# Kernel optimization log

Measured on AMD Instinct MI355X. Metric: run time of the kernel, lower is better.

The kernel has to match this reference:

```python
import jax, jax.numpy as jnp
import numpy as np

B, S, D, H = 2, 2048, 1024, 16
DK = D // H


def setup_inputs() -> dict:
    key = jax.random.key(0)
    ks = jax.random.split(key, 11)
    sc = 0.02
    return {
        "q": jax.random.normal(ks[0], (B, S, D), jnp.float32),
        "k": jax.random.normal(ks[1], (B, S, D), jnp.float32),
        "v": jax.random.normal(ks[2], (B, S, D), jnp.float32),
        "mask": jnp.ones((1, 1, S, S), jnp.int32),
        "w_q": jax.random.normal(ks[3], (D, D), jnp.float32) * sc,
        "b_q": jnp.zeros((D,), jnp.float32),
        "w_k": jax.random.normal(ks[4], (D, D), jnp.float32) * sc,
        "b_k": jnp.zeros((D,), jnp.float32),
        "w_v": jax.random.normal(ks[5], (D, D), jnp.float32) * sc,
        "b_v": jnp.zeros((D,), jnp.float32),
        "w_o": jax.random.normal(ks[6], (D, D), jnp.float32) * sc,
        "b_o": jnp.zeros((D,), jnp.float32),
    }


def reference(q, k, v, mask, w_q, b_q, w_k, b_k, w_v, b_v, w_o, b_o):
    # projections (torch Linear: x @ W.T + b)
    Q = q @ w_q.T + b_q
    K = k @ w_k.T + b_k
    V = v @ w_v.T + b_v
    # [B,S,D] -> [B,H,S,DK]
    Q = Q.reshape(B, S, H, DK).transpose(0, 2, 1, 3)
    K = K.reshape(B, S, H, DK).transpose(0, 2, 1, 3)
    V = V.reshape(B, S, H, DK).transpose(0, 2, 1, 3)
    scores = jnp.einsum('bhqd,bhkd->bhqk', Q, K) / jnp.sqrt(jnp.float32(DK))
    scores = jnp.where(mask == 0, jnp.float32(-1e9), scores)
    attn = jax.nn.softmax(scores, axis=-1)  # dropout p=0.0 -> identity
    X = jnp.einsum('bhqk,bhkd->bhqd', attn, V)
    X = X.transpose(0, 2, 1, 3).reshape(B, S, D)
    return X @ w_o.T + b_o
```

## Files before the change

### kernel.cpp

```cpp
#include <hip/hip_runtime.h>
#include <cstdint>
#include <cstddef>


typedef __attribute__((ext_vector_type(8))) short short8;
typedef __attribute__((ext_vector_type(4))) float float4v;
typedef __attribute__((ext_vector_type(4))) unsigned short us4;

#define DEV __device__ __forceinline__
#define MFMA16(a, b, c) __builtin_amdgcn_mfma_f32_16x16x32_bf16((a), (b), (c), 0, 0, 0)

DEV unsigned short f2bf(float f) {
  union { float f; unsigned u; } c; c.f = f;
  unsigned u = c.u + 0x7fffu + ((c.u >> 16) & 1u);
  return (unsigned short)(u >> 16);
}

DEV void async16(const void* g, void* l) {
  __builtin_amdgcn_global_load_lds(
      (__attribute__((address_space(1))) void*)(uintptr_t)g,
      (__attribute__((address_space(3))) void*)l, 16, 0, 0);
}

struct CvtJob { const float* src; unsigned short* dst; int n; int mode; };
struct CvtArgs { CvtJob job[8]; };

__global__ __launch_bounds__(256) void cvt_bf16_kernel(CvtArgs args) {
  CvtJob j = args.job[blockIdx.y];
  int i = (blockIdx.x * 256 + threadIdx.x) * 8;
  if (i >= j.n) return;
  if (j.mode == 0) {
    float4v a = *(const float4v*)(j.src + i);
    float4v b = *(const float4v*)(j.src + i + 4);
    short8 o;
#pragma unroll
    for (int t = 0; t < 4; ++t) { o[t] = (short)f2bf(a[t]); o[t + 4] = (short)f2bf(b[t]); }
    *(short8*)(j.dst + i) = o;
  } else {
    const int* mi = (const int*)j.src + i;
    int4 a = ((const int4*)mi)[0], b = ((const int4*)mi)[1];
    unsigned bits = (a.x != 0 ? 1u : 0) | (a.y != 0 ? 2u : 0) | (a.z != 0 ? 4u : 0) |
                    (a.w != 0 ? 8u : 0) | (b.x != 0 ? 16u : 0) | (b.y != 0 ? 32u : 0) |
                    (b.z != 0 ? 64u : 0) | (b.w != 0 ? 128u : 0);
    unsigned long long w = (unsigned long long)bits << ((threadIdx.x & 7) * 8);
    w |= __shfl_xor(w, 1);
    w |= __shfl_xor(w, 2);
    w |= __shfl_xor(w, 4);
    if ((threadIdx.x & 7) == 0) ((unsigned long long*)j.dst)[i >> 6] = w;
  }
}

__global__ __launch_bounds__(128) void mask_flags_kernel(const unsigned long long* __restrict__ mb,
                                                         unsigned int* __restrict__ flags) {
  int qb = blockIdx.x >> 5, kt = blockIdx.x & 31;
  int t = threadIdx.x;
  unsigned long long w = mb[(size_t)(qb * 128 + t) * 32 + kt];
  unsigned long long b = __ballot(w == ~0ULL);
  __shared__ unsigned int sh[2];
  if ((t & 63) == 0) sh[t >> 6] = (b == ~0ULL) ? 1u : 0u;
  __syncthreads();
  if (t == 0) flags[blockIdx.x] = sh[0] & sh[1];
}

struct GemmJob {
  const unsigned short* A; const unsigned short* W; const float* bias;
  void* out; float scale; int mode;
};
struct GemmArgs { GemmJob job[3]; };

__global__ __launch_bounds__(256, 2) void gemm128_kernel(GemmArgs args) {
  const GemmJob jb = args.job[blockIdx.z];
  const int tid = threadIdx.x;
  const int wave = tid >> 6, lane = tid & 63, lk = lane & 15, quad = lane >> 4;
  const int wm = wave >> 1, wn = wave & 1;
  const int m0 = blockIdx.y * 128, n0 = blockIdx.x * 128;

  __shared__ unsigned short As[128 * 32];
  __shared__ unsigned short Bs[128 * 32];

  float4v acc[4][4] = {};

  const char* Ag = (const char*)jb.A + (size_t)m0 * 2048;
  const char* Wg = (const char*)jb.W + (size_t)n0 * 2048;

#pragma unroll 1
  for (int kk = 0; kk < 32; ++kk) {
    __syncthreads();
    const int kbyte = kk * 64;
#pragma unroll
    for (int i = 0; i < 2; ++i) {
      int o = (wave * 2 + i) * 1024 + lane * 16;
      int r = o >> 6, cb = o & 63;
      async16(Ag + (size_t)r * 2048 + kbyte + cb, (char*)As + (wave * 2 + i) * 1024);
      async16(Wg + (size_t)r * 2048 + kbyte + cb, (char*)Bs + (wave * 2 + i) * 1024);
    }
    __builtin_amdgcn_s_waitcnt(0);
    __syncthreads();

    short8 af[4];
#pragma unroll
    for (int mt = 0; mt < 4; ++mt)
      af[mt] = *(const short8*)(&As[(wm * 64 + mt * 16 + lk) * 32 + quad * 8]);
#pragma unroll
    for (int nt = 0; nt < 4; ++nt) {
      short8 bf = *(const short8*)(&Bs[(wn * 64 + nt * 16 + lk) * 32 + quad * 8]);
#pragma unroll
      for (int mt = 0; mt < 4; ++mt)
        acc[mt][nt] = MFMA16(af[mt], bf, acc[mt][nt]);
    }
  }

  if (jb.mode == 0) {
    unsigned short* outp = (unsigned short*)jb.out;
#pragma unroll
    for (int nt = 0; nt < 4; ++nt) {
      int n = n0 + wn * 64 + nt * 16 + lk;
      float bn = jb.bias[n];
      int h = n >> 6, d = n & 63;
#pragma unroll
      for (int mt = 0; mt < 4; ++mt) {
#pragma unroll
        for (int r = 0; r < 4; ++r) {
          int m = m0 + wm * 64 + mt * 16 + quad * 4 + r;
          int b = m >> 11, s = m & 2047;
          float v = (acc[mt][nt][r] + bn) * jb.scale;
          outp[((size_t)((b * 16 + h) * 2048 + s) << 6) + d] = f2bf(v);
        }
      }
    }
  } else {
    unsigned short* outp = (unsigned short*)jb.out;
#pragma unroll
    for (int nt = 0; nt < 4; ++nt) {
      int n = n0 + wn * 64 + nt * 16 + lk;
      float bn = jb.bias[n];
      int h = n >> 6, d = n & 63;
#pragma unroll
      for (int mt = 0; mt < 4; ++mt) {
        int m = m0 + wm * 64 + mt * 16 + quad * 4;
        int b = m >> 11, s = m & 2047;
        us4 pk;
#pragma unroll
        for (int r = 0; r < 4; ++r) pk[r] = f2bf(acc[mt][nt][r] + bn);
        *(us4*)(&outp[((size_t)((b * 16 + h) * 64 + d) << 11) + s]) = pk;
      }
    }
  }
}

__global__ __launch_bounds__(256, 2) void gemm_out64_kernel(
    const unsigned short* __restrict__ A, const unsigned short* __restrict__ W,
    const float* __restrict__ bias, float* __restrict__ out) {
  const int tid = threadIdx.x;
  const int wave = tid >> 6, lane = tid & 63, lk = lane & 15, quad = lane >> 4;
  const int wm = wave >> 1, wn = wave & 1;
  const int m0 = blockIdx.y * 64, n0 = blockIdx.x * 128;

  __shared__ unsigned short As[64 * 32];
  __shared__ unsigned short Bs[128 * 32];

  float4v acc[2][4] = {};

  const char* Ag = (const char*)A + (size_t)m0 * 2048;
  const char* Wg = (const char*)W + (size_t)n0 * 2048;

#pragma unroll 1
  for (int kk = 0; kk < 32; ++kk) {
    __syncthreads();
    const int kbyte = kk * 64;
    {
      int o = wave * 1024 + lane * 16;
      int r = o >> 6, cb = o & 63;
      async16(Ag + (size_t)r * 2048 + kbyte + cb, (char*)As + wave * 1024);
    }
#pragma unroll
    for (int i = 0; i < 2; ++i) {
      int o = (wave * 2 + i) * 1024 + lane * 16;
      int r = o >> 6, cb = o & 63;
      async16(Wg + (size_t)r * 2048 + kbyte + cb, (char*)Bs + (wave * 2 + i) * 1024);
    }
    __builtin_amdgcn_s_waitcnt(0);
    __syncthreads();

    short8 af[2];
#pragma unroll
    for (int mt = 0; mt < 2; ++mt)
      af[mt] = *(const short8*)(&As[(wm * 32 + mt * 16 + lk) * 32 + quad * 8]);
#pragma unroll
    for (int nt = 0; nt < 4; ++nt) {
      short8 bf = *(const short8*)(&Bs[(wn * 64 + nt * 16 + lk) * 32 + quad * 8]);
#pragma unroll
      for (int mt = 0; mt < 2; ++mt)
        acc[mt][nt] = MFMA16(af[mt], bf, acc[mt][nt]);
    }
  }

#pragma unroll
  for (int nt = 0; nt < 4; ++nt) {
    int n = n0 + wn * 64 + nt * 16 + lk;
    float bn = bias[n];
#pragma unroll
    for (int mt = 0; mt < 2; ++mt) {
#pragma unroll
      for (int r = 0; r < 4; ++r) {
        int m = m0 + wm * 32 + mt * 16 + quad * 4 + r;
        out[(size_t)m * 1024 + n] = acc[mt][nt][r] + bn;
      }
    }
  }
}

__global__ __launch_bounds__(256, 2) void attn_kernel(
    const unsigned short* __restrict__ Qp, const unsigned short* __restrict__ Kp,
    const unsigned short* __restrict__ Vtp, const unsigned int* __restrict__ flags,
    const unsigned long long* __restrict__ mbits, unsigned short* __restrict__ Xout) {
  __shared__ unsigned short Qs[128 * 64];
  __shared__ unsigned short Ks[2][64 * 64];
  __shared__ unsigned short Vts[2][64 * 64];
  __shared__ unsigned short Ps[128 * 72];
  __shared__ float lsum[128];

  const int tid = threadIdx.x, wave = tid >> 6, lane = tid & 63;
  const int lk = lane & 15, quad = lane >> 4;
  const int bh = blockIdx.y, q0 = blockIdx.x * 128;
  const size_t cbase = (size_t)bh * (2048 * 64);
  const int r8 = lane >> 3, gs = lane & 7;

#pragma unroll
  for (int i = 0; i < 4; ++i) {
    int row = wave * 32 + i * 8 + r8;
    int g = gs ^ (row & 7);
    async16(Qp + cbase + (size_t)(q0 + row) * 64 + g * 8,
            (char*)Qs + (wave * 32 + i * 8) * 128);
  }
#pragma unroll
  for (int i = 0; i < 2; ++i) {
    int row = wave * 16 + i * 8 + r8;
    int g = gs ^ (row & 7);
    async16(Kp + cbase + (size_t)row * 64 + g * 8, (char*)&Ks[0][0] + (wave * 16 + i * 8) * 128);
    async16(Vtp + cbase + (size_t)row * 2048 + g * 8, (char*)&Vts[0][0] + (wave * 16 + i * 8) * 128);
  }
  __builtin_amdgcn_s_waitcnt(0);
  __syncthreads();

  short8 qf[2][2];
#pragma unroll
  for (int mt = 0; mt < 2; ++mt)
#pragma unroll
    for (int ks = 0; ks < 2; ++ks) {
      int row = wave * 32 + mt * 16 + lk;
      int gg = (ks * 4 + quad) ^ (lk & 7);
      qf[mt][ks] = *(const short8*)(&Qs[row * 64 + gg * 8]);
    }

  float rs[8];
#pragma unroll
  for (int i = 0; i < 8; ++i) rs[i] = 0.f;
  float4v O[4][2] = {};

#pragma unroll 1
  for (int kt = 0; kt < 32; ++kt) {
    const int cur = kt & 1;
    if (kt < 31) {
#pragma unroll
      for (int i = 0; i < 2; ++i) {
        int row = wave * 16 + i * 8 + r8;
        int g = gs ^ (row & 7);
        async16(Kp + cbase + (size_t)((kt + 1) * 64 + row) * 64 + g * 8,
                (char*)&Ks[cur ^ 1][0] + (wave * 16 + i * 8) * 128);
        async16(Vtp + cbase + (size_t)row * 2048 + (kt + 1) * 64 + g * 8,
                (char*)&Vts[cur ^ 1][0] + (wave * 16 + i * 8) * 128);
      }
    }

    float4v sacc[2][4] = {};
#pragma unroll
    for (int nt = 0; nt < 4; ++nt) {
      int krow = nt * 16 + lk;
      short8 kb0 = *(const short8*)(&Ks[cur][krow * 64 + ((quad) ^ (lk & 7)) * 8]);
      short8 kb1 = *(const short8*)(&Ks[cur][krow * 64 + ((4 + quad) ^ (lk & 7)) * 8]);
#pragma unroll
      for (int mt = 0; mt < 2; ++mt) {
        sacc[mt][nt] = MFMA16(qf[mt][0], kb0, sacc[mt][nt]);
        sacc[mt][nt] = MFMA16(qf[mt][1], kb1, sacc[mt][nt]);
      }
    }

    if (__builtin_expect(flags[blockIdx.x * 32 + kt] == 0, 0)) {
#pragma unroll
      for (int i = 0; i < 8; ++i) {
        int row = q0 + wave * 32 + (i >> 2) * 16 + quad * 4 + (i & 3);
        unsigned long long w = mbits[(size_t)row * 32 + kt];
#pragma unroll
        for (int nt = 0; nt < 4; ++nt)
          if (!((w >> (nt * 16 + lk)) & 1ULL))
            sacc[i >> 2][nt][i & 3] = -__builtin_inff();
      }
    }

#pragma unroll
    for (int mt = 0; mt < 2; ++mt)
#pragma unroll
      for (int nt = 0; nt < 4; ++nt)
#pragma unroll
        for (int r = 0; r < 4; ++r) {
          float p = __expf(sacc[mt][nt][r]);
          unsigned pu = __float_as_uint(p);
          rs[mt * 4 + r] += __uint_as_float(pu & 0xffff0000u);
          Ps[(wave * 32 + mt * 16 + quad * 4 + r) * 72 + nt * 16 + lk] =
              (unsigned short)(pu >> 16);
        }

    short8 pb[2][2];
#pragma unroll
    for (int qt = 0; qt < 2; ++qt)
#pragma unroll
      for (int ks = 0; ks < 2; ++ks)
        pb[qt][ks] = *(const short8*)(&Ps[(wave * 32 + qt * 16 + lk) * 72 + ks * 32 + quad * 8]);
#pragma unroll
    for (int dt = 0; dt < 4; ++dt) {
      int drow = dt * 16 + lk;
      short8 va0 = *(const short8*)(&Vts[cur][drow * 64 + ((quad) ^ (lk & 7)) * 8]);
      short8 va1 = *(const short8*)(&Vts[cur][drow * 64 + ((4 + quad) ^ (lk & 7)) * 8]);
#pragma unroll
      for (int qt = 0; qt < 2; ++qt) {
        O[dt][qt] = MFMA16(va0, pb[qt][0], O[dt][qt]);
        O[dt][qt] = MFMA16(va1, pb[qt][1], O[dt][qt]);
      }
    }

    __builtin_amdgcn_s_waitcnt(0x0f70);
    __syncthreads();
  }

#pragma unroll
  for (int i = 0; i < 8; ++i) {
    float s = rs[i];
    s += __shfl_xor(s, 1); s += __shfl_xor(s, 2);
    s += __shfl_xor(s, 4); s += __shfl_xor(s, 8);
    rs[i] = s;
  }
  if (lk == 0) {
#pragma unroll
    for (int i = 0; i < 8; ++i)
      lsum[wave * 32 + (i >> 2) * 16 + quad * 4 + (i & 3)] = rs[i];
  }
  __syncthreads();
  float linv[2];
#pragma unroll
  for (int qt = 0; qt < 2; ++qt) linv[qt] = 1.f / lsum[wave * 32 + qt * 16 + lk];

  const int b = bh >> 4, h = bh & 15;
#pragma unroll
  for (int dt = 0; dt < 4; ++dt)
#pragma unroll
    for (int qt = 0; qt < 2; ++qt) {
      int s = q0 + wave * 32 + qt * 16 + lk;
      us4 pk;
#pragma unroll
      for (int rr = 0; rr < 4; ++rr) pk[rr] = f2bf(O[dt][qt][rr] * linv[qt]);
      *(us4*)(&Xout[((size_t)(b * 2048 + s)) * 1024 + h * 64 + dt * 16 + quad * 4]) = pk;
    }
}

extern "C" void kernel_launch(void* const* d_in, const int* in_sizes, int n_in,
                              void* d_out, int out_size, void* d_ws, size_t ws_size,
                              hipStream_t stream) {
  const float* q   = (const float*)d_in[0];
  const float* k   = (const float*)d_in[1];
  const float* v   = (const float*)d_in[2];
  const int*   msk = (const int*)d_in[3];
  const float* w_q = (const float*)d_in[4];
  const float* b_q = (const float*)d_in[5];
  const float* w_k = (const float*)d_in[6];
  const float* b_k = (const float*)d_in[7];
  const float* w_v = (const float*)d_in[8];
  const float* b_v = (const float*)d_in[9];
  const float* w_o = (const float*)d_in[10];
  const float* b_o = (const float*)d_in[11];

  char* ws = (char*)d_ws;
  const size_t MB = (size_t)1 << 20;
  unsigned short* q_bf  = (unsigned short*)(ws + 0 * MB);
  unsigned short* k_bf  = (unsigned short*)(ws + 8 * MB);
  unsigned short* v_bf  = (unsigned short*)(ws + 16 * MB);
  unsigned short* wq_bf = (unsigned short*)(ws + 24 * MB);
  unsigned short* wk_bf = (unsigned short*)(ws + 26 * MB);
  unsigned short* wv_bf = (unsigned short*)(ws + 28 * MB);
  unsigned short* wo_bf = (unsigned short*)(ws + 30 * MB);
  unsigned short* Qp    = (unsigned short*)(ws + 32 * MB);
  unsigned short* Kp    = (unsigned short*)(ws + 40 * MB);
  unsigned short* Vtp   = (unsigned short*)(ws + 48 * MB);
  unsigned short* Xa    = (unsigned short*)(ws + 56 * MB);
  unsigned long long* mb = (unsigned long long*)(ws + 64 * MB);
  unsigned int* mflags   = (unsigned int*)(ws + 64 * MB + (512 << 10));

  CvtArgs ca;
  ca.job[0] = { q,   q_bf,  4096 * 1024, 0 };
  ca.job[1] = { k,   k_bf,  4096 * 1024, 0 };
  ca.job[2] = { v,   v_bf,  4096 * 1024, 0 };
  ca.job[3] = { w_q, wq_bf, 1024 * 1024, 0 };
  ca.job[4] = { w_k, wk_bf, 1024 * 1024, 0 };
  ca.job[5] = { w_v, wv_bf, 1024 * 1024, 0 };
  ca.job[6] = { w_o, wo_bf, 1024 * 1024, 0 };
  ca.job[7] = { (const float*)msk, (unsigned short*)mb, 2048 * 2048, 1 };
  cvt_bf16_kernel<<<dim3(2048, 8), 256, 0, stream>>>(ca);

  mask_flags_kernel<<<dim3(512), 128, 0, stream>>>(mb, mflags);

  GemmArgs ga;
  ga.job[0] = { q_bf, wq_bf, b_q, (void*)Qp,  0.125f, 0 };
  ga.job[1] = { k_bf, wk_bf, b_k, (void*)Kp,  1.0f,   0 };
  ga.job[2] = { v_bf, wv_bf, b_v, (void*)Vtp, 1.0f,   2 };
  gemm128_kernel<<<dim3(8, 32, 3), 256, 0, stream>>>(ga);

  attn_kernel<<<dim3(16, 32), 256, 0, stream>>>(Qp, Kp, Vtp, mflags, mb, Xa);

  gemm_out64_kernel<<<dim3(8, 64), 256, 0, stream>>>(Xa, wo_bf, b_o, (float*)d_out);
}
```

Before: 254.6 us.

## Shrink attention Q tile to 64 rows, single-buffer K/V, raise occupancy

The attention kernel now processes 64 query rows per block instead of 128, doubling the grid. K and V tiles are single-buffered, and the launch bound asks for 4 blocks per CU to hide latency through occupancy rather than through software prefetch. The MFMA operand orientation is swapped so each lane owns a query column, which makes the row-sum reduction a pair of shuffles instead of an LDS pass. The mask-flag kernel moves to 64-row granularity to match. The trade-offs are twice the K/V global traffic, no load/compute overlap inside a block, and output written as scalar 2-byte stores.

```diff
diff --git a/kernel.cpp b/kernel.cpp
--- a/kernel.cpp
+++ b/kernel.cpp
@@ -50,16 +50,12 @@
   }
 }
 
-__global__ __launch_bounds__(128) void mask_flags_kernel(const unsigned long long* __restrict__ mb,
-                                                         unsigned int* __restrict__ flags) {
+__global__ __launch_bounds__(64) void mask_flags_kernel(const unsigned long long* __restrict__ mb,
+                                                        unsigned int* __restrict__ flags) {
   int qb = blockIdx.x >> 5, kt = blockIdx.x & 31;
-  int t = threadIdx.x;
-  unsigned long long w = mb[(size_t)(qb * 128 + t) * 32 + kt];
+  unsigned long long w = mb[(size_t)(qb * 64 + threadIdx.x) * 32 + kt];
   unsigned long long b = __ballot(w == ~0ULL);
-  __shared__ unsigned int sh[2];
-  if ((t & 63) == 0) sh[t >> 6] = (b == ~0ULL) ? 1u : 0u;
-  __syncthreads();
-  if (t == 0) flags[blockIdx.x] = sh[0] & sh[1];
+  if (threadIdx.x == 0) flags[blockIdx.x] = (b == ~0ULL) ? 1u : 0u;
 }
 
 struct GemmJob {
@@ -210,156 +206,120 @@
   }
 }
 
-__global__ __launch_bounds__(256, 2) void attn_kernel(
+__global__ __launch_bounds__(256, 4) void attn_kernel(
     const unsigned short* __restrict__ Qp, const unsigned short* __restrict__ Kp,
     const unsigned short* __restrict__ Vtp, const unsigned int* __restrict__ flags,
     const unsigned long long* __restrict__ mbits, unsigned short* __restrict__ Xout) {
-  __shared__ unsigned short Qs[128 * 64];
-  __shared__ unsigned short Ks[2][64 * 64];
-  __shared__ unsigned short Vts[2][64 * 64];
-  __shared__ unsigned short Ps[128 * 72];
-  __shared__ float lsum[128];
+  __shared__ unsigned short Qs[64 * 64];
+  __shared__ unsigned short Ks[64 * 64];
+  __shared__ unsigned short Vts[64 * 64];
+  __shared__ unsigned short Ps[64 * 72];
 
   const int tid = threadIdx.x, wave = tid >> 6, lane = tid & 63;
   const int lk = lane & 15, quad = lane >> 4;
-  const int bh = blockIdx.y, q0 = blockIdx.x * 128;
+  const int bh = blockIdx.y, q0 = blockIdx.x * 64;
   const size_t cbase = (size_t)bh * (2048 * 64);
   const int r8 = lane >> 3, gs = lane & 7;
-
-#pragma unroll
-  for (int i = 0; i < 4; ++i) {
-    int row = wave * 32 + i * 8 + r8;
-    int g = gs ^ (row & 7);
-    async16(Qp + cbase + (size_t)(q0 + row) * 64 + g * 8,
-            (char*)Qs + (wave * 32 + i * 8) * 128);
-  }
+  const int sw = lk & 7;
+
 #pragma unroll
   for (int i = 0; i < 2; ++i) {
     int row = wave * 16 + i * 8 + r8;
     int g = gs ^ (row & 7);
-    async16(Kp + cbase + (size_t)row * 64 + g * 8, (char*)&Ks[0][0] + (wave * 16 + i * 8) * 128);
-    async16(Vtp + cbase + (size_t)row * 2048 + g * 8, (char*)&Vts[0][0] + (wave * 16 + i * 8) * 128);
-  }
-  __builtin_amdgcn_s_waitcnt(0);
-  __syncthreads();
-
-  short8 qf[2][2];
-#pragma unroll
-  for (int mt = 0; mt < 2; ++mt)
-#pragma unroll
-    for (int ks = 0; ks < 2; ++ks) {
-      int row = wave * 32 + mt * 16 + lk;
-      int gg = (ks * 4 + quad) ^ (lk & 7);
-      qf[mt][ks] = *(const short8*)(&Qs[row * 64 + gg * 8]);
-    }
-
-  float rs[8];
-#pragma unroll
-  for (int i = 0; i < 8; ++i) rs[i] = 0.f;
-  float4v O[4][2] = {};
+    async16(Qp + cbase + (size_t)(q0 + row) * 64 + g * 8,
+            (char*)Qs + (wave * 16 + i * 8) * 128);
+  }
+  __builtin_amdgcn_s_waitcnt(0x0f70);
+
+  short8 qf[2];
+#pragma unroll
+  for (int ks = 0; ks < 2; ++ks) {
+    int row = wave * 16 + lk;
+    int gg = (ks * 4 + quad) ^ (row & 7);
+    qf[ks] = *(const short8*)(&Qs[row * 64 + gg * 8]);
+  }
+
+  float rsum = 0.f;
+  float4v O[4] = {};
 
 #pragma unroll 1
   for (int kt = 0; kt < 32; ++kt) {
-    const int cur = kt & 1;
-    if (kt < 31) {
-#pragma unroll
-      for (int i = 0; i < 2; ++i) {
-        int row = wave * 16 + i * 8 + r8;
-        int g = gs ^ (row & 7);
-        async16(Kp + cbase + (size_t)((kt + 1) * 64 + row) * 64 + g * 8,
-                (char*)&Ks[cur ^ 1][0] + (wave * 16 + i * 8) * 128);
-        async16(Vtp + cbase + (size_t)row * 2048 + (kt + 1) * 64 + g * 8,
-                (char*)&Vts[cur ^ 1][0] + (wave * 16 + i * 8) * 128);
+    __syncthreads();
+#pragma unroll
+    for (int i = 0; i < 2; ++i) {
+      int row = wave * 16 + i * 8 + r8;
+      int g = gs ^ (row & 7);
+      async16(Kp + cbase + (size_t)(kt * 64 + row) * 64 + g * 8,
+              (char*)Ks + (wave * 16 + i * 8) * 128);
+      async16(Vtp + cbase + (size_t)row * 2048 + kt * 64 + g * 8,
+              (char*)Vts + (wave * 16 + i * 8) * 128);
+    }
+    __builtin_amdgcn_s_waitcnt(0x0f70);
+    __syncthreads();
+
+    float4v sacc[4] = {};
+#pragma unroll
+    for (int kt4 = 0; kt4 < 4; ++kt4) {
+      int krow = kt4 * 16 + lk;
+      short8 ka0 = *(const short8*)(&Ks[krow * 64 + ((quad) ^ sw) * 8]);
+      short8 ka1 = *(const short8*)(&Ks[krow * 64 + ((4 + quad) ^ sw) * 8]);
+      sacc[kt4] = MFMA16(ka0, qf[0], sacc[kt4]);
+      sacc[kt4] = MFMA16(ka1, qf[1], sacc[kt4]);
+    }
+
+    if (__builtin_expect(flags[blockIdx.x * 32 + kt] == 0, 0)) {
+      unsigned long long w = mbits[(size_t)(q0 + wave * 16 + lk) * 32 + kt];
+#pragma unroll
+      for (int kt4 = 0; kt4 < 4; ++kt4)
+#pragma unroll
+        for (int r = 0; r < 4; ++r)
+          if (!((w >> (kt4 * 16 + quad * 4 + r)) & 1ULL))
+            sacc[kt4][r] = -__builtin_inff();
+    }
+
+#pragma unroll
+    for (int kt4 = 0; kt4 < 4; ++kt4) {
+      us4 pk;
+#pragma unroll
+      for (int r = 0; r < 4; ++r) {
+        float p = __expf(sacc[kt4][r]);
+        unsigned pu = __float_as_uint(p);
+        rsum += __uint_as_float(pu & 0xffff0000u);
+        pk[r] = (unsigned short)(pu >> 16);
       }
-    }
-
-    float4v sacc[2][4] = {};
-#pragma unroll
-    for (int nt = 0; nt < 4; ++nt) {
-      int krow = nt * 16 + lk;
-      short8 kb0 = *(const short8*)(&Ks[cur][krow * 64 + ((quad) ^ (lk & 7)) * 8]);
-      short8 kb1 = *(const short8*)(&Ks[cur][krow * 64 + ((4 + quad) ^ (lk & 7)) * 8]);
-#pragma unroll
-      for (int mt = 0; mt < 2; ++mt) {
-        sacc[mt][nt] = MFMA16(qf[mt][0], kb0, sacc[mt][nt]);
-        sacc[mt][nt] = MFMA16(qf[mt][1], kb1, sacc[mt][nt]);
-      }
-    }
-
-    if (__builtin_expect(flags[blockIdx.x * 32 + kt] == 0, 0)) {
-#pragma unroll
-      for (int i = 0; i < 8; ++i) {
-        int row = q0 + wave * 32 + (i >> 2) * 16 + quad * 4 + (i & 3);
-        unsigned long long w = mbits[(size_t)row * 32 + kt];
-#pragma unroll
-        for (int nt = 0; nt < 4; ++nt)
-          if (!((w >> (nt * 16 + lk)) & 1ULL))
-            sacc[i >> 2][nt][i & 3] = -__builtin_inff();
-      }
-    }
-
-#pragma unroll
-    for (int mt = 0; mt < 2; ++mt)
-#pragma unroll
-      for (int nt = 0; nt < 4; ++nt)
-#pragma unroll
-        for (int r = 0; r < 4; ++r) {
-          float p = __expf(sacc[mt][nt][r]);
-          unsigned pu = __float_as_uint(p);
-          rs[mt * 4 + r] += __uint_as_float(pu & 0xffff0000u);
-          Ps[(wave * 32 + mt * 16 + quad * 4 + r) * 72 + nt * 16 + lk] =
-              (unsigned short)(pu >> 16);
-        }
-
-    short8 pb[2][2];
-#pragma unroll
-    for (int qt = 0; qt < 2; ++qt)
-#pragma unroll
-      for (int ks = 0; ks < 2; ++ks)
-        pb[qt][ks] = *(const short8*)(&Ps[(wave * 32 + qt * 16 + lk) * 72 + ks * 32 + quad * 8]);
+      *(us4*)(&Ps[(wave * 16 + lk) * 72 + kt4 * 16 + quad * 4]) = pk;
+    }
+
+    short8 pa[2];
+#pragma unroll
+    for (int ks = 0; ks < 2; ++ks)
+      pa[ks] = *(const short8*)(&Ps[(wave * 16 + lk) * 72 + ks * 32 + quad * 8]);
 #pragma unroll
     for (int dt = 0; dt < 4; ++dt) {
       int drow = dt * 16 + lk;
-      short8 va0 = *(const short8*)(&Vts[cur][drow * 64 + ((quad) ^ (lk & 7)) * 8]);
-      short8 va1 = *(const short8*)(&Vts[cur][drow * 64 + ((4 + quad) ^ (lk & 7)) * 8]);
-#pragma unroll
-      for (int qt = 0; qt < 2; ++qt) {
-        O[dt][qt] = MFMA16(va0, pb[qt][0], O[dt][qt]);
-        O[dt][qt] = MFMA16(va1, pb[qt][1], O[dt][qt]);
-      }
-    }
-
-    __builtin_amdgcn_s_waitcnt(0x0f70);
-    __syncthreads();
-  }
-
-#pragma unroll
-  for (int i = 0; i < 8; ++i) {
-    float s = rs[i];
-    s += __shfl_xor(s, 1); s += __shfl_xor(s, 2);
-    s += __shfl_xor(s, 4); s += __shfl_xor(s, 8);
-    rs[i] = s;
-  }
-  if (lk == 0) {
-#pragma unroll
-    for (int i = 0; i < 8; ++i)
-      lsum[wave * 32 + (i >> 2) * 16 + quad * 4 + (i & 3)] = rs[i];
-  }
-  __syncthreads();
-  float linv[2];
-#pragma unroll
-  for (int qt = 0; qt < 2; ++qt) linv[qt] = 1.f / lsum[wave * 32 + qt * 16 + lk];
+      short8 vb0 = *(const short8*)(&Vts[drow * 64 + ((quad) ^ sw) * 8]);
+      short8 vb1 = *(const short8*)(&Vts[drow * 64 + ((4 + quad) ^ sw) * 8]);
+      O[dt] = MFMA16(pa[0], vb0, O[dt]);
+      O[dt] = MFMA16(pa[1], vb1, O[dt]);
+    }
+  }
+
+  float s = rsum;
+  s += __shfl_xor(s, 16);
+  s += __shfl_xor(s, 32);
+  float inv = 1.f / s;
+  float linv[4];
+#pragma unroll
+  for (int r = 0; r < 4; ++r) linv[r] = __shfl(inv, (wave << 6 & 0) + quad * 4 + r);
 
   const int b = bh >> 4, h = bh & 15;
 #pragma unroll
   for (int dt = 0; dt < 4; ++dt)
 #pragma unroll
-    for (int qt = 0; qt < 2; ++qt) {
-      int s = q0 + wave * 32 + qt * 16 + lk;
-      us4 pk;
-#pragma unroll
-      for (int rr = 0; rr < 4; ++rr) pk[rr] = f2bf(O[dt][qt][rr] * linv[qt]);
-      *(us4*)(&Xout[((size_t)(b * 2048 + s)) * 1024 + h * 64 + dt * 16 + quad * 4]) = pk;
+    for (int r = 0; r < 4; ++r) {
+      int qq = q0 + wave * 16 + quad * 4 + r;
+      int d = dt * 16 + lk;
+      Xout[((size_t)(b * 2048 + qq)) * 1024 + h * 64 + d] = f2bf(O[dt][r] * linv[r]);
     }
 }
 
@@ -406,7 +366,7 @@
   ca.job[7] = { (const float*)msk, (unsigned short*)mb, 2048 * 2048, 1 };
   cvt_bf16_kernel<<<dim3(2048, 8), 256, 0, stream>>>(ca);
 
-  mask_flags_kernel<<<dim3(512), 128, 0, stream>>>(mb, mflags);
+  mask_flags_kernel<<<dim3(1024), 64, 0, stream>>>(mb, mflags);
 
   GemmArgs ga;
   ga.job[0] = { q_bf, wq_bf, b_q, (void*)Qp,  0.125f, 0 };
@@ -414,7 +374,7 @@
   ga.job[2] = { v_bf, wv_bf, b_v, (void*)Vtp, 1.0f,   2 };
   gemm128_kernel<<<dim3(8, 32, 3), 256, 0, stream>>>(ga);
 
-  attn_kernel<<<dim3(16, 32), 256, 0, stream>>>(Qp, Kp, Vtp, mflags, mb, Xa);
+  attn_kernel<<<dim3(32, 32), 256, 0, stream>>>(Qp, Kp, Vtp, mflags, mb, Xa);
 
   gemm_out64_kernel<<<dim3(8, 64), 256, 0, stream>>>(Xa, wo_bf, b_o, (float*)d_out);
 }
```

Result: faster. 247.7 us (-2.7%).
